# Performance work log

Measured on AMD Instinct MI355X. Metric: run time of the kernel, lower is better.

Reference implementation:

```python
import jax, jax.numpy as jnp
from jax import lax
import numpy as np

B, S, D = 64, 512, 256
VOCAB, NC = 50000, 10
N_STEPS = 10  # ode_step=11 points -> 10 intervals, h=0.1
BN_EPS = 1e-5


def setup_inputs() -> dict:
    key = jax.random.key(0)
    ks = jax.random.split(key, 16)
    inp = {}
    inp['input_ids'] = jax.random.randint(ks[0], (B, S), 0, VOCAB)
    inp['emb'] = jax.random.normal(ks[1], (VOCAB, D), dtype=jnp.float32)
    inp['W_ode'] = 0.1 * jax.random.normal(ks[2], (D, D), dtype=jnp.float32)  # init std=0.1
    inp['b_ode'] = jnp.zeros((D,), dtype=jnp.float32)
    for i, kk in enumerate([3, 4, 5]):
        fan_in = D * kk
        inp[f'w{kk}'] = jax.random.normal(ks[3 + 3 * i], (128, D, kk), jnp.float32) / np.sqrt(fan_in)
        inp[f'b{kk}'] = jax.random.normal(ks[4 + 3 * i], (128,), jnp.float32) * 0.01
        inp[f'g{kk}'] = jnp.ones((128,), jnp.float32)
        inp[f'be{kk}'] = jnp.zeros((128,), jnp.float32)
    inp['wc'] = jax.random.normal(ks[12], (NC, D + 3 * 128), jnp.float32) / np.sqrt(D + 3 * 128)
    inp['bc'] = jnp.zeros((NC,), jnp.float32)
    return inp


def _forward(input_ids, emb, W_ode, b_ode, w3, b3, g3, be3, w4, b4, g4, be4,
             w5, b5, g5, be5, wc, bc):
    x = emb[input_ids]                      # (B,S,D)
    # --- Neural ODE branch: linear RHS f(z) = z W^T + b, RK4 fixed-step on [0,1] ---
    z0 = x.reshape(-1, D)                   # (B*S, D)
    h = jnp.float32(1.0 / N_STEPS)

    def f(z):
        return z @ W_ode.T + b_ode

    def step(z, _):
        k1 = f(z)
        k2 = f(z + 0.5 * h * k1)
        k3 = f(z + 0.5 * h * k2)
        k4 = f(z + h * k3)
        return z + (h / 6.0) * (k1 + 2 * k2 + 2 * k3 + k4), None

    z, _ = lax.scan(step, z0, None, length=N_STEPS)
    node_pooled = z.reshape(B, S, D).max(axis=1)   # global max over seq -> (B,D)

    # --- TextCNN branches on raw embeddings ---
    cin = jnp.transpose(x, (0, 2, 1))       # (B,D,S)
    inv_std = jnp.float32(1.0 / np.sqrt(1.0 + BN_EPS))  # BN eval: mean=0, var=1

    def branch(w, b, g, be):
        c = lax.conv_general_dilated(cin, w, (1,), 'VALID',
                                     dimension_numbers=('NCH', 'OIH', 'NCH'))
        c = c + b[None, :, None]
        c = g[None, :, None] * (c * inv_std) + be[None, :, None]
        c = jax.nn.relu(c)
        return c.max(axis=2)                # (B,128)

    p3 = branch(w3, b3, g3, be3)
    p4 = branch(w4, b4, g4, be4)
    p5 = branch(w5, b5, g5, be5)

    feats = jnp.concatenate([node_pooled, p3, p4, p5], axis=1)  # (B,640)
    return feats @ wc.T + bc                # (B,NC); dropout is identity in eval


def reference(input_ids, emb, W_ode, b_ode, w3, b3, g3, be3, w4, b4, g4, be4,
              w5, b5, g5, be5, wc, bc):
    return _forward(input_ids, emb, W_ode, b_ode, w3, b3, g3, be3,
                    w4, b4, g4, be4, w5, b5, g5, be5, wc, bc)
```

## Files before the change

kernel.cpp:

```cpp
#include <hip/hip_runtime.h>


typedef short bf16x8 __attribute__((ext_vector_type(8)));
typedef float f32x4 __attribute__((ext_vector_type(4)));

__device__ __forceinline__ unsigned short f2bf(float f) {
  unsigned u = __float_as_uint(f);
  u += 0x7FFFu + ((u >> 16) & 1u);
  return (unsigned short)(u >> 16);
}

__device__ __forceinline__ float dotcol64(const float* __restrict__ xrow,
                                          const float* __restrict__ Y, int c) {
  float a0 = 0.f, a1 = 0.f, a2 = 0.f, a3 = 0.f;
#pragma unroll 1
  for (int w = 0; w < 4; ++w) {
    float bv[64];
#pragma unroll
    for (int v = 0; v < 64; ++v) bv[v] = Y[(w * 64 + v) * 256 + c];
#pragma unroll
    for (int v = 0; v < 64; v += 4) {
      a0 = fmaf(xrow[w * 64 + v + 0], bv[v + 0], a0);
      a1 = fmaf(xrow[w * 64 + v + 1], bv[v + 1], a1);
      a2 = fmaf(xrow[w * 64 + v + 2], bv[v + 2], a2);
      a3 = fmaf(xrow[w * 64 + v + 3], bv[v + 3], a3);
    }
  }
  return (a0 + a1) + (a2 + a3);
}

__global__ __launch_bounds__(256) void k_prep1(
    const float* __restrict__ W, const float* __restrict__ bode,
    const float* __restrict__ w3c, const float* __restrict__ w4c, const float* __restrict__ w5c,
    float* __restrict__ Bm, float* __restrict__ c1,
    unsigned short* __restrict__ slab, unsigned* __restrict__ featbuf) {
  __shared__ float r1[256], r2[256], r3[256], red[4];
  const int tid = threadIdx.x, blk = blockIdx.x;
  if (blk < 256) {
    const int i = blk;
    r1[tid] = W[i * 256 + tid];
    __syncthreads();
    const float v2 = dotcol64(r1, W, tid);
    r2[tid] = v2;
    __syncthreads();
    const float v3 = dotcol64(r2, W, tid);
    r3[tid] = v3;
    __syncthreads();
    const float v4 = dotcol64(r3, W, tid);
    const float w1 = r1[tid];
    Bm[i * 256 + tid] = 0.1f * w1 + 0.005f * v2
                      + (0.001f / 6.f) * v3 + (0.0001f / 24.f) * v4;
    const float q = 0.05f * w1 + (0.01f / 6.f) * v2 + (0.001f / 24.f) * v3;
    float val = bode[tid] * q;
#pragma unroll
    for (int off = 32; off > 0; off >>= 1) val += __shfl_down(val, off);
    if ((tid & 63) == 0) red[tid >> 6] = val;
    __syncthreads();
    if (tid == 0) c1[i] = 0.1f * (bode[i] + ((red[0] + red[1]) + (red[2] + red[3])));
  } else {
    const int base = (blk - 256) * 256 + tid;
#pragma unroll
    for (int u = 0; u < 4; ++u) {
      int e = base + u * 98304;
      int s = e >> 15, r = e & 32767, kd = r >> 7, o = r & 127;
      const float* w; int k, j;
      if (s < 3)      { w = w3c; k = 3; j = s; }
      else if (s < 7) { w = w4c; k = 4; j = s - 3; }
      else            { w = w5c; k = 5; j = s - 7; }
      float val = w[(o * 256 + kd) * k + j];
      int kc = kd >> 5, quad = (kd >> 3) & 3, q8 = kd & 7;
      slab[s * 32768 + ((kc * 4 + quad) * 128 + o) * 8 + q8] = f2bf(val);
    }
    if (base < 64 * 640) featbuf[base] = 0u;
  }
}

__global__ __launch_bounds__(256) void k_prep2(
    const float* __restrict__ Bm, const float* __restrict__ c1v,
    float* __restrict__ c10, unsigned short* __restrict__ slab) {
  __shared__ float curs[256], c1s[256], red[4];
  const int tid = threadIdx.x, i = blockIdx.x;
  const float coefN[11] = {1.f, 10.f, 45.f, 120.f, 210.f, 252.f,
                           210.f, 120.f, 45.f, 10.f, 1.f};
  float v = Bm[i * 256 + tid];
  curs[tid] = v;
  c1s[tid] = c1v[tid];
  float n10 = ((i == tid) ? 1.f : 0.f) + 10.f * v;
  float pd = v * c1s[tid];
#pragma unroll
  for (int off = 32; off > 0; off >>= 1) pd += __shfl_down(pd, off);
  if ((tid & 63) == 0) red[tid >> 6] = pd;
  __syncthreads();
  float ct = 10.f * c1s[i] + 45.f * ((red[0] + red[1]) + (red[2] + red[3]));

#pragma unroll 1
  for (int k = 2; k <= 10; ++k) {
    v = dotcol64(curs, Bm, tid);
    n10 = fmaf(coefN[k], v, n10);
    float pdk = v * c1s[tid];
#pragma unroll
    for (int off = 32; off > 0; off >>= 1) pdk += __shfl_down(pdk, off);
    if ((tid & 63) == 0) red[tid >> 6] = pdk;
    __syncthreads();
    if (k <= 9) {
      ct = fmaf(coefN[k + 1], (red[0] + red[1]) + (red[2] + red[3]), ct);
    }
    curs[tid] = v;
    __syncthreads();
  }

  {
    const int o = i, kd = tid;
    const int kc = kd >> 5, quad = (kd >> 3) & 3, q8 = kd & 7;
    slab[(12 + (o >> 7)) * 32768 + ((kc * 4 + quad) * 128 + (o & 127)) * 8 + q8] = f2bf(n10);
  }
  if (tid == 0) c10[i] = ct;
}


__global__ __launch_bounds__(256, 2) void k_main(
    const int* __restrict__ ids, const float* __restrict__ emb,
    const unsigned short* __restrict__ slab, const float* __restrict__ ctot,
    const float* __restrict__ b3, const float* __restrict__ g3, const float* __restrict__ be3,
    const float* __restrict__ b4, const float* __restrict__ g4, const float* __restrict__ be4,
    const float* __restrict__ b5, const float* __restrict__ g5, const float* __restrict__ be5,
    unsigned* __restrict__ featbuf) {
  __shared__ alignas(16) unsigned short Xt[68 * 264];
  __shared__ int ids_s[68];
  const int tid = threadIdx.x;
  const int blk = blockIdx.x;
  const int b = blk >> 3;
  const int t0 = (blk & 7) * 64;
  const int lane = tid & 63;
  const int wave = tid >> 6;
  const int m15 = lane & 15;
  const int quad = lane >> 4;

  if (tid < 68) {
    int t = t0 + tid;
    ids_s[tid] = (t < 512) ? ids[b * 512 + t] : -1;
  }
  __syncthreads();
  for (int i = tid; i < 68 * 64; i += 256) {
    int row = i >> 6, s4 = i & 63;
    uint2 v = make_uint2(0u, 0u);
    int id = ids_s[row];
    if (id >= 0) {
      const float4 f = *(const float4*)(emb + (size_t)id * 256 + s4 * 4);
      v.x = (unsigned)f2bf(f.x) | ((unsigned)f2bf(f.y) << 16);
      v.y = (unsigned)f2bf(f.z) | ((unsigned)f2bf(f.w) << 16);
    }
    *(uint2*)&Xt[row * 264 + s4 * 4] = v;
  }
  __syncthreads();

  const unsigned short* fb0 = slab + ((size_t)quad * 128 + (wave * 2 + 0) * 16 + m15) * 8;
  const unsigned short* fb1 = fb0 + 128;

  bf16x8 fA[4], fB[4];
#pragma unroll
  for (int q = 0; q < 4; ++q) {
    fA[q] = *(const bf16x8*)(((q & 1) ? fb1 : fb0) + (q >> 1) * 4096);
    fB[q] = *(const bf16x8*)(((q & 1) ? fb1 : fb0) + 8192 + (q >> 1) * 4096);
  }

  f32x4 acc[4][2];
#pragma unroll
  for (int mt = 0; mt < 4; ++mt)
#pragma unroll
    for (int nt = 0; nt < 2; ++nt) acc[mt][nt] = (f32x4){0.f, 0.f, 0.f, 0.f};

#define ENTRY(KCQ, FR)                                                          \
  {                                                                             \
    _Pragma("unroll")                                                           \
    for (int kc2 = 0; kc2 < 2; ++kc2) {                                         \
      const int kd0 = ((KCQ) * 2 + kc2) * 32 + quad * 8;                        \
      bf16x8 af[4];                                                             \
      _Pragma("unroll")                                                         \
      for (int mt = 0; mt < 4; ++mt)                                            \
        af[mt] = *(const bf16x8*)&Xt[(shift + mt * 16 + m15) * 264 + kd0];      \
      _Pragma("unroll")                                                         \
      for (int mt = 0; mt < 4; ++mt) {                                          \
        acc[mt][0] = __builtin_amdgcn_mfma_f32_16x16x32_bf16(af[mt], FR[kc2 * 2 + 0], acc[mt][0], 0, 0, 0); \
        acc[mt][1] = __builtin_amdgcn_mfma_f32_16x16x32_bf16(af[mt], FR[kc2 * 2 + 1], acc[mt][1], 0, 0, 0); \
      }                                                                         \
    }                                                                           \
  }

  for (int ep = 0; ep < 28; ++ep) {
    const int e0 = ep * 2;
    const int slice = e0 >> 2;
    const int shift = (slice < 3) ? slice
                    : (slice < 7) ? (slice - 3)
                    : (slice < 12) ? (slice - 7) : 0;
    const int kcq0 = e0 & 3;

    ENTRY(kcq0, fA);
    if (ep < 27) {
      const int eo = (e0 + 2) * 8192;
#pragma unroll
      for (int q = 0; q < 4; ++q)
        fA[q] = *(const bf16x8*)(((q & 1) ? fb1 : fb0) + eo + (q >> 1) * 4096);
    }
    ENTRY(kcq0 + 1, fB);
    if (ep < 27) {
      const int eo = (e0 + 3) * 8192;
#pragma unroll
      for (int q = 0; q < 4; ++q)
        fB[q] = *(const bf16x8*)(((q & 1) ? fb1 : fb0) + eo + (q >> 1) * 4096);
    }

    const int g = (ep == 5) ? 0 : (ep == 13) ? 1 : (ep == 23) ? 2
                : (ep == 25) ? 3 : (ep == 27) ? 4 : -1;
    if (g >= 0) {
      if (g < 3) {
        const int kk = g + 3;
        const float* bb  = (g == 0) ? b3 : (g == 1) ? b4 : b5;
        const float* gg  = (g == 0) ? g3 : (g == 1) ? g4 : g5;
        const float* bbe = (g == 0) ? be3 : (g == 1) ? be4 : be5;
        const int off = 256 + g * 128;
        const int tmax = 512 - kk;
#pragma unroll
        for (int nt = 0; nt < 2; ++nt) {
          const int n = (wave * 2 + nt) * 16 + m15;
          const float sc = gg[n] * 0.9999950000375f;
          const float sh = fmaf(sc, bb[n], bbe[n]);
          float mx = 0.f;
#pragma unroll
          for (int mt = 0; mt < 4; ++mt)
#pragma unroll
            for (int r = 0; r < 4; ++r) {
              const int t = t0 + mt * 16 + quad * 4 + r;
              const float v = fmaf(sc, acc[mt][nt][r], sh);
              if (t <= tmax) mx = fmaxf(mx, v);
            }
          mx = fmaxf(mx, __shfl_xor(mx, 16));
          mx = fmaxf(mx, __shfl_xor(mx, 32));
          if (quad == 0) atomicMax(&featbuf[b * 640 + off + n], __float_as_uint(mx));
        }
      } else {
        const int base = (g == 3) ? 0 : 128;
#pragma unroll
        for (int nt = 0; nt < 2; ++nt) {
          const int n = (wave * 2 + nt) * 16 + m15;
          const float ct = ctot[base + n];
          float mx = -3.4e38f;
#pragma unroll
          for (int mt = 0; mt < 4; ++mt)
#pragma unroll
            for (int r = 0; r < 4; ++r)
              mx = fmaxf(mx, acc[mt][nt][r] + ct);
          mx = fmaxf(mx, __shfl_xor(mx, 16));
          mx = fmaxf(mx, __shfl_xor(mx, 32));
          if (quad == 0) {
            unsigned bits = __float_as_uint(mx);
            unsigned key = (bits & 0x80000000u) ? ~bits : (bits | 0x80000000u);
            atomicMax(&featbuf[b * 640 + base + n], key);
          }
        }
      }
#pragma unroll
      for (int mt = 0; mt < 4; ++mt)
#pragma unroll
        for (int nt = 0; nt < 2; ++nt) acc[mt][nt] = (f32x4){0.f, 0.f, 0.f, 0.f};
    }
  }
#undef ENTRY
}

__global__ void k_fin(const unsigned* __restrict__ featbuf, const float* __restrict__ wc,
                      const float* __restrict__ bc, float* __restrict__ out) {
  int b = blockIdx.x, lane = threadIdx.x;
  float p[10];
#pragma unroll
  for (int c = 0; c < 10; ++c) p[c] = 0.f;
  for (int f = lane; f < 640; f += 64) {
    unsigned u = featbuf[b * 640 + f];
    float v;
    if (f < 256) v = (u & 0x80000000u) ? __uint_as_float(u ^ 0x80000000u) : __uint_as_float(~u);
    else v = __uint_as_float(u);
#pragma unroll
    for (int c = 0; c < 10; ++c) p[c] = fmaf(v, wc[c * 640 + f], p[c]);
  }
#pragma unroll
  for (int c = 0; c < 10; ++c) {
    float s = p[c];
#pragma unroll
    for (int off = 32; off > 0; off >>= 1) s += __shfl_down(s, off);
    if (lane == 0) out[b * 10 + c] = s + bc[c];
  }
}

extern "C" void kernel_launch(void* const* d_in, const int* in_sizes, int n_in,
                              void* d_out, int out_size, void* d_ws, size_t ws_size,
                              hipStream_t stream) {
  (void)in_sizes; (void)n_in; (void)out_size; (void)ws_size;
  const int*   ids  = (const int*)d_in[0];
  const float* emb  = (const float*)d_in[1];
  const float* W    = (const float*)d_in[2];
  const float* bode = (const float*)d_in[3];
  const float* w3   = (const float*)d_in[4];
  const float* b3   = (const float*)d_in[5];
  const float* g3   = (const float*)d_in[6];
  const float* be3  = (const float*)d_in[7];
  const float* w4   = (const float*)d_in[8];
  const float* b4   = (const float*)d_in[9];
  const float* g4   = (const float*)d_in[10];
  const float* be4  = (const float*)d_in[11];
  const float* w5   = (const float*)d_in[12];
  const float* b5   = (const float*)d_in[13];
  const float* g5   = (const float*)d_in[14];
  const float* be5  = (const float*)d_in[15];
  const float* wc   = (const float*)d_in[16];
  const float* bc   = (const float*)d_in[17];
  float* out = (float*)d_out;

  float* wsf = (float*)d_ws;
  float* Bm  = wsf;
  float* c1  = wsf + 65536;
  float* c10 = wsf + 65792;
  unsigned short* slab = (unsigned short*)(wsf + 66048);
  unsigned* featbuf = (unsigned*)(wsf + 295424);

  hipLaunchKernelGGL(k_prep1, dim3(640), dim3(256), 0, stream,
                     W, bode, w3, w4, w5, Bm, c1, slab, featbuf);
  hipLaunchKernelGGL(k_prep2, dim3(256), dim3(256), 0, stream, Bm, c1, c10, slab);
  hipLaunchKernelGGL(k_main, dim3(512), dim3(256), 0, stream,
                     ids, emb, slab, c10,
                     b3, g3, be3, b4, g4, be4, b5, g5, be5, featbuf);
  hipLaunchKernelGGL(k_fin, dim3(64), dim3(64), 0, stream, featbuf, wc, bc, out);
}
```

Baseline: 200.1 us.

## Factor ODE matrix power via squared step and deepen main-loop fragment prefetch

The ten-step propagator (I+B)^10 is now built as ((I+B)^2)^5. A new kernel forms D = 2B + B^2 and the matching bias term, then a second kernel computes the fifth power with binomial coefficients. This shortens the serial chain of 256x256 matrix-vector products from nine to five, at the cost of one extra kernel launch. The main kernel now keeps four weight-fragment register sets in flight instead of two, issues the first global loads before the embedding gather, and reorders the conv-weight slab transpose indexing. More live registers may reduce occupancy.

```diff
diff --git a/kernel.cpp b/kernel.cpp
--- a/kernel.cpp
+++ b/kernel.cpp
@@ -62,7 +62,8 @@
 #pragma unroll
     for (int u = 0; u < 4; ++u) {
       int e = base + u * 98304;
-      int s = e >> 15, r = e & 32767, kd = r >> 7, o = r & 127;
+      int s = e >> 15, r = e & 32767;
+      int o = r >> 8, kd = r & 255;
       const float* w; int k, j;
       if (s < 3)      { w = w3c; k = 3; j = s; }
       else if (s < 7) { w = w4c; k = 4; j = s - 3; }
@@ -75,38 +76,55 @@
   }
 }
 
-__global__ __launch_bounds__(256) void k_prep2(
+__global__ __launch_bounds__(256) void k_prep2a(
     const float* __restrict__ Bm, const float* __restrict__ c1v,
-    float* __restrict__ c10, unsigned short* __restrict__ slab) {
-  __shared__ float curs[256], c1s[256], red[4];
+    float* __restrict__ Dm, float* __restrict__ c1b) {
+  __shared__ float r1[256], c1s[256], red[4];
   const int tid = threadIdx.x, i = blockIdx.x;
-  const float coefN[11] = {1.f, 10.f, 45.f, 120.f, 210.f, 252.f,
-                           210.f, 120.f, 45.f, 10.f, 1.f};
-  float v = Bm[i * 256 + tid];
-  curs[tid] = v;
+  r1[tid] = Bm[i * 256 + tid];
   c1s[tid] = c1v[tid];
-  float n10 = ((i == tid) ? 1.f : 0.f) + 10.f * v;
-  float pd = v * c1s[tid];
+  __syncthreads();
+  const float v2 = dotcol64(r1, Bm, tid);
+  Dm[i * 256 + tid] = 2.f * r1[tid] + v2;
+  float pd = r1[tid] * c1s[tid];
 #pragma unroll
   for (int off = 32; off > 0; off >>= 1) pd += __shfl_down(pd, off);
   if ((tid & 63) == 0) red[tid >> 6] = pd;
   __syncthreads();
-  float ct = 10.f * c1s[i] + 45.f * ((red[0] + red[1]) + (red[2] + red[3]));
+  if (tid == 0) c1b[i] = 2.f * c1s[i] + ((red[0] + red[1]) + (red[2] + red[3]));
+}
+
+__global__ __launch_bounds__(256) void k_prep2b(
+    const float* __restrict__ Dm, const float* __restrict__ c1bv,
+    float* __restrict__ c10, unsigned short* __restrict__ slab) {
+  __shared__ float curs[256], cbs[256], red[4];
+  const int tid = threadIdx.x, i = blockIdx.x;
+  const float coefN[6] = {1.f, 5.f, 10.f, 10.f, 5.f, 1.f};
+  const float coefC[5] = {5.f, 10.f, 10.f, 5.f, 1.f};
+  float v = Dm[i * 256 + tid];
+  curs[tid] = v;
+  cbs[tid] = c1bv[tid];
+  __syncthreads();
+  float n10 = ((i == tid) ? 1.f : 0.f) + coefN[1] * v;
+  float pd = v * cbs[tid];
+#pragma unroll
+  for (int off = 32; off > 0; off >>= 1) pd += __shfl_down(pd, off);
+  if ((tid & 63) == 0) red[tid >> 6] = pd;
+  __syncthreads();
+  float ct = coefC[0] * cbs[i] + coefC[1] * ((red[0] + red[1]) + (red[2] + red[3]));
 
 #pragma unroll 1
-  for (int k = 2; k <= 10; ++k) {
-    v = dotcol64(curs, Bm, tid);
+  for (int k = 2; k <= 5; ++k) {
+    v = dotcol64(curs, Dm, tid);
+    __syncthreads();
+    curs[tid] = v;
     n10 = fmaf(coefN[k], v, n10);
-    float pdk = v * c1s[tid];
+    float pdk = v * cbs[tid];
 #pragma unroll
     for (int off = 32; off > 0; off >>= 1) pdk += __shfl_down(pdk, off);
     if ((tid & 63) == 0) red[tid >> 6] = pdk;
     __syncthreads();
-    if (k <= 9) {
-      ct = fmaf(coefN[k + 1], (red[0] + red[1]) + (red[2] + red[3]), ct);
-    }
-    curs[tid] = v;
-    __syncthreads();
+    if (k <= 4) ct = fmaf(coefC[k], (red[0] + red[1]) + (red[2] + red[3]), ct);
   }
 
   {
@@ -141,6 +159,19 @@
     ids_s[tid] = (t < 512) ? ids[b * 512 + t] : -1;
   }
   __syncthreads();
+
+  const unsigned short* fb0 = slab + ((size_t)quad * 128 + wave * 2 * 16 + m15) * 8;
+  bf16x8 fA[4], fB[4], fC[4], fD[4];
+#define LDFRAG(DST, EN)                                                         \
+  {                                                                             \
+    const unsigned short* p_ = fb0 + (EN) * 8192;                               \
+    DST[0] = *(const bf16x8*)(p_);                                              \
+    DST[1] = *(const bf16x8*)(p_ + 128);                                        \
+    DST[2] = *(const bf16x8*)(p_ + 4096);                                       \
+    DST[3] = *(const bf16x8*)(p_ + 4096 + 128);                                 \
+  }
+  LDFRAG(fA, 0) LDFRAG(fB, 1) LDFRAG(fC, 2) LDFRAG(fD, 3)
+
   for (int i = tid; i < 68 * 64; i += 256) {
     int row = i >> 6, s4 = i & 63;
     uint2 v = make_uint2(0u, 0u);
@@ -153,16 +184,6 @@
     *(uint2*)&Xt[row * 264 + s4 * 4] = v;
   }
   __syncthreads();
-
-  const unsigned short* fb0 = slab + ((size_t)quad * 128 + (wave * 2 + 0) * 16 + m15) * 8;
-  const unsigned short* fb1 = fb0 + 128;
-
-  bf16x8 fA[4], fB[4];
-#pragma unroll
-  for (int q = 0; q < 4; ++q) {
-    fA[q] = *(const bf16x8*)(((q & 1) ? fb1 : fb0) + (q >> 1) * 4096);
-    fB[q] = *(const bf16x8*)(((q & 1) ? fb1 : fb0) + 8192 + (q >> 1) * 4096);
-  }
 
   f32x4 acc[4][2];
 #pragma unroll
@@ -187,31 +208,16 @@
     }                                                                           \
   }
 
-  for (int ep = 0; ep < 28; ++ep) {
-    const int e0 = ep * 2;
-    const int slice = e0 >> 2;
-    const int shift = (slice < 3) ? slice
-                    : (slice < 7) ? (slice - 3)
-                    : (slice < 12) ? (slice - 7) : 0;
-    const int kcq0 = e0 & 3;
-
-    ENTRY(kcq0, fA);
-    if (ep < 27) {
-      const int eo = (e0 + 2) * 8192;
-#pragma unroll
-      for (int q = 0; q < 4; ++q)
-        fA[q] = *(const bf16x8*)(((q & 1) ? fb1 : fb0) + eo + (q >> 1) * 4096);
-    }
-    ENTRY(kcq0 + 1, fB);
-    if (ep < 27) {
-      const int eo = (e0 + 3) * 8192;
-#pragma unroll
-      for (int q = 0; q < 4; ++q)
-        fB[q] = *(const bf16x8*)(((q & 1) ? fb1 : fb0) + eo + (q >> 1) * 4096);
-    }
-
-    const int g = (ep == 5) ? 0 : (ep == 13) ? 1 : (ep == 23) ? 2
-                : (ep == 25) ? 3 : (ep == 27) ? 4 : -1;
+  for (int eq = 0; eq < 14; ++eq) {
+    const int shift = (eq < 3) ? eq : (eq < 7) ? (eq - 3) : (eq < 12) ? (eq - 7) : 0;
+
+    ENTRY(0, fA) if (eq < 13) LDFRAG(fA, (eq + 1) * 4 + 0)
+    ENTRY(1, fB) if (eq < 13) LDFRAG(fB, (eq + 1) * 4 + 1)
+    ENTRY(2, fC) if (eq < 13) LDFRAG(fC, (eq + 1) * 4 + 2)
+    ENTRY(3, fD) if (eq < 13) LDFRAG(fD, (eq + 1) * 4 + 3)
+
+    const int g = (eq == 2) ? 0 : (eq == 6) ? 1 : (eq == 11) ? 2
+                : (eq == 12) ? 3 : (eq == 13) ? 4 : -1;
     if (g >= 0) {
       if (g < 3) {
         const int kk = g + 3;
@@ -266,6 +272,7 @@
     }
   }
 #undef ENTRY
+#undef LDFRAG
 }
 
 __global__ void k_fin(const unsigned* __restrict__ featbuf, const float* __restrict__ wc,
@@ -317,14 +324,17 @@
 
   float* wsf = (float*)d_ws;
   float* Bm  = wsf;
-  float* c1  = wsf + 65536;
-  float* c10 = wsf + 65792;
-  unsigned short* slab = (unsigned short*)(wsf + 66048);
-  unsigned* featbuf = (unsigned*)(wsf + 295424);
+  float* Dm  = wsf + 65536;
+  float* c1  = wsf + 131072;
+  float* c1b = wsf + 131328;
+  float* c10 = wsf + 131584;
+  unsigned short* slab = (unsigned short*)(wsf + 131840);
+  unsigned* featbuf = (unsigned*)(wsf + 361216);
 
   hipLaunchKernelGGL(k_prep1, dim3(640), dim3(256), 0, stream,
                      W, bode, w3, w4, w5, Bm, c1, slab, featbuf);
-  hipLaunchKernelGGL(k_prep2, dim3(256), dim3(256), 0, stream, Bm, c1, c10, slab);
+  hipLaunchKernelGGL(k_prep2a, dim3(256), dim3(256), 0, stream, Bm, c1, Dm, c1b);
+  hipLaunchKernelGGL(k_prep2b, dim3(256), dim3(256), 0, stream, Dm, c1b, c10, slab);
   hipLaunchKernelGGL(k_main, dim3(512), dim3(256), 0, stream,
                      ids, emb, slab, c10,
                      b3, g3, be3, b4, g4, be4, b5, g5, be5, featbuf);
```

New measurement: 195.7 us. 2.2% less time.
